# Kernel tuning notes

Hardware: AMD Instinct MI355X
Metric: run time of the kernel (lower is better)

Reference implementation:

```python
import jax, jax.numpy as jnp
import numpy as np

# ---- static config (mirrors ProposalLayerModule param) ----
FEAT_STRIDE = 16
PRE_NMS_TOPN = 6000
POST_NMS_TOPN = 300
NMS_THRESH = 0.7
MIN_SIZE = 16.0
NUM_ANCHORS = 9


def _generate_anchors():
    """Replicates generate_anchors(base_size=16, ratios=[0.5,1,2], scales=[8,16,32])."""
    base = np.array([0.0, 0.0, 15.0, 15.0])
    ratios = np.array([0.5, 1.0, 2.0])
    scales = np.array([8.0, 16.0, 32.0])
    w = base[2] - base[0] + 1.0
    h = base[3] - base[1] + 1.0
    xc = base[0] + 0.5 * (w - 1.0)
    yc = base[1] + 0.5 * (h - 1.0)
    size = w * h
    ws = np.round(np.sqrt(size / ratios))
    hs = np.round(ws * ratios)
    ratio_anchors = np.stack([xc - 0.5 * (ws - 1), yc - 0.5 * (hs - 1),
                              xc + 0.5 * (ws - 1), yc + 0.5 * (hs - 1)], axis=1)
    out = []
    for a in ratio_anchors:
        aw = a[2] - a[0] + 1.0
        ah = a[3] - a[1] + 1.0
        axc = a[0] + 0.5 * (aw - 1.0)
        ayc = a[1] + 0.5 * (ah - 1.0)
        ws2 = aw * scales
        hs2 = ah * scales
        out.append(np.stack([axc - 0.5 * (ws2 - 1), ayc - 0.5 * (hs2 - 1),
                             axc + 0.5 * (ws2 - 1), ayc + 0.5 * (hs2 - 1)], axis=1))
    return np.concatenate(out, axis=0).astype(np.float32)  # (9, 4)

_ANCHORS = _generate_anchors()


def _nms_keep(iou, valid, thresh):
    """Greedy NMS over score-sorted boxes. Returns boolean keep mask."""
    n = iou.shape[0]
    idx = jnp.arange(n)
    def body(i, keep):
        sup = keep[i] & (iou[i] > thresh) & (idx > i)
        return keep & jnp.logical_not(sup)
    return jax.lax.fori_loop(0, n, body, valid)


def setup_inputs() -> dict:
    key = jax.random.key(0)
    k1, k2 = jax.random.split(key)
    H, W = 128, 192
    scores = jax.random.normal(k1, (1, 2 * NUM_ANCHORS, H, W), dtype=jnp.float32)
    # small deltas so exp(dw), exp(dh) stay in a realistic range
    bbox_deltas = jax.random.normal(k2, (1, 4 * NUM_ANCHORS, H, W), dtype=jnp.float32) * 0.1
    im_info = jnp.array([H * FEAT_STRIDE, W * FEAT_STRIDE, 1.0], dtype=jnp.float32)
    return {"scores": scores, "bbox_deltas": bbox_deltas, "im_info": im_info}


def reference(scores, bbox_deltas, im_info):
    A = NUM_ANCHORS
    s = scores[0, A:]                      # (A, H, W) fg scores
    Hf, Wf = s.shape[1], s.shape[2]
    # shifts, matching torch.meshgrid default indexing='ij' (x-major flatten)
    shift_x = jnp.arange(Wf, dtype=jnp.float32) * FEAT_STRIDE
    shift_y = jnp.arange(Hf, dtype=jnp.float32) * FEAT_STRIDE
    sx, sy = jnp.meshgrid(shift_x, shift_y, indexing='ij')   # (W, H)
    shifts = jnp.stack([sx.ravel(), sy.ravel(), sx.ravel(), sy.ravel()], axis=1)  # (K,4)
    anchors = (jnp.asarray(_ANCHORS)[None, :, :] + shifts[:, None, :]).reshape(-1, 4)  # (K*A,4)

    deltas = jnp.transpose(bbox_deltas[0], (1, 2, 0)).reshape(-1, 4)  # (H*W*A,4)
    sc = jnp.transpose(s, (1, 2, 0)).reshape(-1)                      # (H*W*A,)

    # bbox_transform_inv
    widths = anchors[:, 2] - anchors[:, 0] + 1.0
    heights = anchors[:, 3] - anchors[:, 1] + 1.0
    ctr_x = anchors[:, 0] + 0.5 * widths
    ctr_y = anchors[:, 1] + 0.5 * heights
    dx, dy, dw, dh = deltas[:, 0], deltas[:, 1], deltas[:, 2], deltas[:, 3]
    pcx = dx * widths + ctr_x
    pcy = dy * heights + ctr_y
    pw = jnp.exp(dw) * widths
    ph = jnp.exp(dh) * heights
    x1 = pcx - 0.5 * pw
    y1 = pcy - 0.5 * ph
    x2 = pcx + 0.5 * pw
    y2 = pcy + 0.5 * ph

    # clip_boxes
    x1 = jnp.clip(x1, 0.0, im_info[1] - 1.0)
    x2 = jnp.clip(x2, 0.0, im_info[1] - 1.0)
    y1 = jnp.clip(y1, 0.0, im_info[0] - 1.0)
    y2 = jnp.clip(y2, 0.0, im_info[0] - 1.0)
    boxes = jnp.stack([x1, y1, x2, y2], axis=1)

    # _filter_boxes (as a mask, jit-friendly)
    ms = MIN_SIZE * im_info[2]
    valid = ((x2 - x1 + 1.0) >= ms) & ((y2 - y1 + 1.0) >= ms)
    masked_sc = jnp.where(valid, sc, -jnp.inf)

    # sort by score descending + pre_nms_topN
    top_s, top_i = jax.lax.top_k(masked_sc, PRE_NMS_TOPN)
    b = boxes[top_i]                       # (PRE, 4), score-sorted
    vld = jnp.isfinite(top_s)

    # torchvision-style IoU (no +1) + greedy NMS
    area = (b[:, 2] - b[:, 0]) * (b[:, 3] - b[:, 1])
    ix1 = jnp.maximum(b[:, None, 0], b[None, :, 0])
    iy1 = jnp.maximum(b[:, None, 1], b[None, :, 1])
    ix2 = jnp.minimum(b[:, None, 2], b[None, :, 2])
    iy2 = jnp.minimum(b[:, None, 3], b[None, :, 3])
    inter = jnp.clip(ix2 - ix1, 0.0) * jnp.clip(iy2 - iy1, 0.0)
    iou = inter / jnp.maximum(area[:, None] + area[None, :] - inter, 1e-9)
    keep = _nms_keep(iou, vld, NMS_THRESH)

    # first post_nms_topN kept boxes (fixed-size, zero-padded), prepend batch idx 0
    cum = jnp.cumsum(keep.astype(jnp.int32))
    pos = jnp.where(keep & (cum <= POST_NMS_TOPN), cum - 1, POST_NMS_TOPN)
    rows = jnp.concatenate([jnp.zeros((PRE_NMS_TOPN, 1), jnp.float32), b], axis=1)
    out = jnp.zeros((POST_NMS_TOPN + 1, 5), jnp.float32).at[pos].set(rows)[:POST_NMS_TOPN]
    return out
```

## Files before the change

kernel.cpp:

```cpp
#include <hip/hip_runtime.h>

#define NCELL 24576
#define NTOT  221184
#define NBIN13 8192
#define TOPN  6000
#define POSTN 300
#define NPADR 6016
#define NW    94
#define CW    8
#define NCHUNK 12
#define NCB   16
#define SLOT  1024
#define CAP2  (NCB*SLOT)

__global__ void decode_kernel(const float* __restrict__ scores,
                              const float* __restrict__ deltas,
                              const float* __restrict__ iminfo,
                              float4* __restrict__ boxes,
                              unsigned* __restrict__ skeys) {
#pragma clang fp contract(off)
    int c = blockIdx.x * blockDim.x + threadIdx.x;
    if (c >= NCELL) return;
    const float AW[9] = {184.f,368.f,736.f,128.f,256.f,512.f, 88.f,176.f,352.f};
    const float AH[9] = { 96.f,192.f,384.f,128.f,256.f,512.f,176.f,352.f,704.f};
    float sx = (float)((c >> 7) << 4);
    float sy = (float)((c & 127) << 4);
    float imh = iminfo[0], imw = iminfo[1], ims = iminfo[2];
    float xhi = imw - 1.0f, yhi = imh - 1.0f;
    float ms = 16.0f * ims;
    float ctrx = sx + 8.0f, ctry = sy + 8.0f;
    const float* sbase = scores + 9 * NCELL + c;
    const float* dbase = deltas + c;
#pragma unroll
    for (int a = 0; a < 9; ++a) {
        float sc = sbase[a * NCELL];
        float dx = dbase[(4 * a + 0) * NCELL];
        float dy = dbase[(4 * a + 1) * NCELL];
        float dw = dbase[(4 * a + 2) * NCELL];
        float dh = dbase[(4 * a + 3) * NCELL];
        float pcx = dx * AW[a] + ctrx;
        float pcy = dy * AH[a] + ctry;
        float pw = expf(dw) * AW[a];
        float ph = expf(dh) * AH[a];
        float x1 = pcx - 0.5f * pw;
        float y1 = pcy - 0.5f * ph;
        float x2 = pcx + 0.5f * pw;
        float y2 = pcy + 0.5f * ph;
        x1 = fminf(fmaxf(x1, 0.0f), xhi);
        x2 = fminf(fmaxf(x2, 0.0f), xhi);
        y1 = fminf(fmaxf(y1, 0.0f), yhi);
        y2 = fminf(fmaxf(y2, 0.0f), yhi);
        bool valid = ((x2 - x1 + 1.0f) >= ms) && ((y2 - y1 + 1.0f) >= ms);
        unsigned u = __float_as_uint(sc);
        unsigned key = (u & 0x80000000u) ? ~u : (u | 0x80000000u);
        if (!valid) key = 0x007FFFFFu;
        boxes[a * NCELL + c] = make_float4(x1, y1, x2, y2);
        skeys[a * NCELL + c] = key;
    }
}

__global__ __launch_bounds__(1024) void compactT_kernel(const unsigned* __restrict__ skeys,
                                                        unsigned* __restrict__ meta16,
                                                        unsigned long long* __restrict__ cbuf) {
    __shared__ unsigned hist[NBIN13];
    __shared__ unsigned psum[1024];
    __shared__ unsigned csum[256];
    __shared__ unsigned sB, sAbove, sT, sCount;
    int tid = threadIdx.x, bid = blockIdx.x;
    for (int b = tid; b < NBIN13; b += 1024) hist[b] = 0u;
    if (tid == 0) sCount = 0u;
    __syncthreads();
    const uint4* s4 = (const uint4*)skeys;
    for (int q = tid; q < NTOT / 4; q += 1024) {
        uint4 u = s4[q];
        atomicAdd(&hist[u.x >> 19], 1u);
        atomicAdd(&hist[u.y >> 19], 1u);
        atomicAdd(&hist[u.z >> 19], 1u);
        atomicAdd(&hist[u.w >> 19], 1u);
    }
    __syncthreads();
    unsigned s = 0;
#pragma unroll
    for (int q = 0; q < 8; ++q) s += hist[tid * 8 + q];
    psum[tid] = s;
    __syncthreads();
    if (tid < 256)
        csum[tid] = psum[tid * 4] + psum[tid * 4 + 1] + psum[tid * 4 + 2] + psum[tid * 4 + 3];
    __syncthreads();
    if (tid < 64) {
        int lane = tid;
        unsigned c0 = csum[lane * 4 + 0], c1 = csum[lane * 4 + 1];
        unsigned c2 = csum[lane * 4 + 2], c3 = csum[lane * 4 + 3];
        unsigned ls = c0 + c1 + c2 + c3;
        unsigned v = ls;
#pragma unroll
        for (int o = 1; o < 64; o <<= 1) {
            unsigned t = __shfl_down(v, o, 64);
            if (lane + o < 64) v += t;
        }
        unsigned sufExcl = v - ls;
        unsigned a3 = sufExcl;
        unsigned a2 = a3 + c3;
        unsigned a1 = a2 + c2;
        unsigned a0 = a1 + c1;
        if (a0 < TOPN && a0 + c0 >= TOPN) { sB = lane * 4 + 0; sAbove = a0; }
        if (a1 < TOPN && a1 + c1 >= TOPN) { sB = lane * 4 + 1; sAbove = a1; }
        if (a2 < TOPN && a2 + c2 >= TOPN) { sB = lane * 4 + 2; sAbove = a2; }
        if (a3 < TOPN && a3 + c3 >= TOPN) { sB = lane * 4 + 3; sAbove = a3; }
    }
    __syncthreads();
    if (tid < 32) {
        unsigned B = sB, above = sAbove;
        unsigned h = hist[B * 32 + tid];
        unsigned v = h;
#pragma unroll
        for (int o = 1; o < 32; o <<= 1) {
            unsigned t = __shfl_down(v, o, 64);
            if (tid + o < 32) v += t;
        }
        unsigned sufExcl = v - h;
        unsigned ab = above + sufExcl;
        if (ab < TOPN && ab + h >= TOPN) sT = B * 32 + tid;
    }
    __syncthreads();
    unsigned T = sT;
    int base = bid * (NTOT / NCB);
    const uint4* s4b = (const uint4*)(skeys + base);
    for (int q = tid; q < (NTOT / NCB) / 4; q += 1024) {
        uint4 u = s4b[q];
        unsigned k4[4] = {u.x, u.y, u.z, u.w};
#pragma unroll
        for (int k = 0; k < 4; ++k) {
            if ((k4[k] >> 19) >= T) {
                unsigned lp = atomicAdd(&sCount, 1u);
                if (lp < SLOT) {
                    int m = base + 4 * q + k;
                    unsigned n = (unsigned)((m % NCELL) * 9 + (m / NCELL));
                    cbuf[(bid << 10) + lp] =
                        ((unsigned long long)k4[k] << 32) | (unsigned long long)(~n);
                }
            }
        }
    }
    __syncthreads();
    unsigned cnt = sCount; if (cnt > SLOT) cnt = SLOT;
    for (int e = cnt + tid; e < SLOT; e += 1024) cbuf[(bid << 10) + e] = 0ULL;
    if (tid == 0) meta16[bid] = cnt;
}

__global__ __launch_bounds__(256) void rankscatter_kernel(const unsigned long long* __restrict__ cbuf,
                                                          const unsigned* __restrict__ meta16,
                                                          const float4* __restrict__ boxes,
                                                          float4* __restrict__ sortedbox) {
    __shared__ unsigned long long jk[512];
    __shared__ unsigned scnt[NCB];
    int tid = threadIdx.x;
    if (tid < NCB) scnt[tid] = meta16[tid];
    __syncthreads();
    int i = blockIdx.x * 32 + (tid >> 3);
    int slice = tid & 7;
    unsigned long long ki = cbuf[i];
    unsigned cr = 0;
    for (int jt = 0; jt < CAP2 / 512; ++jt) {
        int b = jt >> 1;
        unsigned cb = scnt[b];
        if ((jt & 1) ? (cb <= 512u) : (cb == 0u)) continue;
        __syncthreads();
        for (int q = tid; q < 512; q += 256) jk[q] = cbuf[(jt << 9) + q];
        __syncthreads();
#pragma unroll 8
        for (int j = 0; j < 64; ++j) cr += (jk[slice + (j << 3)] > ki) ? 1u : 0u;
    }
    cr += __shfl_down(cr, 4, 8);
    cr += __shfl_down(cr, 2, 8);
    cr += __shfl_down(cr, 1, 8);
    if (slice == 0 && ki != 0ULL && cr < NPADR) {
        unsigned n = ~(unsigned)ki;
        unsigned m = (n % 9u) * (unsigned)NCELL + (n / 9u);
        sortedbox[cr] = boxes[m];
    }
}

__global__ __launch_bounds__(256) void matrix_kernel(const float4* __restrict__ sortedbox,
                                                     unsigned long long* __restrict__ rowr,
                                                     unsigned long long* __restrict__ diagw,
                                                     unsigned long long* __restrict__ diagT) {
#pragma clang fp contract(off)
    __shared__ float4 jb[256];
    __shared__ float  ja[256];
    int tid = threadIdx.x;
    int lane = tid & 63, wave = tid >> 6;
    int i0 = blockIdx.y << 6;
    int i = i0 + lane;
    int w = (blockIdx.x << 2) + wave;
    int jbase = blockIdx.x << 8;
    unsigned long long word = 0ULL;

    if (jbase + 255 > i0) {
        int jg = jbase + tid;
        float4 v = (jg < NPADR) ? sortedbox[jg] : make_float4(0.f, 0.f, 0.f, 0.f);
        jb[tid] = v;
        ja[tid] = (v.z - v.x) * (v.w - v.y);
        __syncthreads();
        if (w < NW && ((w << 6) + 63) > i) {
            float4 bi = sortedbox[i];
            float ai = (bi.z - bi.x) * (bi.w - bi.y);
            int jl0 = wave << 6;
            int jg0 = (w << 6);
#pragma unroll 8
            for (int j = 0; j < 64; ++j) {
                float4 bj = jb[jl0 + j];
                float aj = ja[jl0 + j];
                float iw = fminf(bi.z, bj.z) - fmaxf(bi.x, bj.x);
                float ih = fminf(bi.w, bj.w) - fmaxf(bi.y, bj.y);
                iw = fmaxf(iw, 0.0f);
                ih = fmaxf(ih, 0.0f);
                float inter = iw * ih;
                float denom = fmaxf(ai + aj - inter, 1e-9f);
                bool sup = (jg0 + j > i) && (inter / denom > 0.7f);
                word |= (unsigned long long)sup << j;
            }
        }
    }
    if (w < NW) {
        rowr[(size_t)i * NW + w] = word;
        if ((i >> 9) == (w >> 3))
            diagw[((size_t)w << 9) + (i & 511)] = word;
        if (w == (i >> 6)) {
            unsigned long long col = 0ULL;
#pragma unroll
            for (int jbit = 0; jbit < 64; ++jbit) {
                unsigned long long m = __ballot((word >> jbit) & 1ULL);
                if (lane == jbit) col = m;
            }
            diagT[((size_t)w << 6) + lane] = col;
        }
    }
}

__global__ __launch_bounds__(256) void scan_kernel(const unsigned long long* __restrict__ rowr,
                                                   const unsigned long long* __restrict__ diagw,
                                                   const unsigned long long* __restrict__ diagT,
                                                   const float4* __restrict__ sortedbox,
                                                   float* __restrict__ out) {
    __shared__ __align__(16) unsigned long long cblk[2][CW * 512];
    __shared__ unsigned long long ldsT[2][CW * 64];
    __shared__ unsigned long long gm[128];
    __shared__ int keptArr[POSTN];
    __shared__ int s_kept, s_done;
    int tid = threadIdx.x;
    int lane = tid & 63, wave = tid >> 6;

    if (tid < 128) gm[tid] = (tid == 93) ? ~((1ULL << 48) - 1) : 0ULL;
    if (tid == 0) { s_kept = 0; s_done = 0; }
    for (int e = tid; e < CW * 512; e += 256) cblk[0][e] = diagw[e];
    for (int e = tid; e < CW * 64; e += 256) ldsT[0][e] = diagT[e];
    __syncthreads();

    int keptPrev = 0;
    for (int c = 0; c < NCHUNK; ++c) {
        int buf = c & 1, nbuf = buf ^ 1;
        int wbase = c * CW;
        if (wave == 0) {
            unsigned long long dgT[CW];
#pragma unroll
            for (int q = 0; q < CW; ++q) dgT[q] = ldsT[buf][(q << 6) + lane];
            unsigned long long lowmask = (1ULL << lane) - 1ULL;
            int kept = s_kept;
            int done = 0;
            for (int q = 0; q < CW && wbase + q < NW; ++q) {
                int w = wbase + q;
                unsigned long long live = ~gm[w];
                if (w == NW - 1) live &= (1ULL << 48) - 1;
                if (!live) continue;
                bool alive = (live >> lane) & 1ULL;
                unsigned long long x = live;
                for (;;) {
                    bool sup = (dgT[q] & x & lowmask) != 0ULL;
                    unsigned long long xn = __ballot(alive && !sup);
                    if (xn == x) break;
                    x = xn;
                }
                unsigned long long kb = x;
                if (kb) {
                    int nk = __popcll(kb);
                    int myr = __popcll(kb & lowmask);
                    if (((kb >> lane) & 1ULL) && (kept + myr < POSTN))
                        keptArr[kept + myr] = (w << 6) + lane;
                    kept += nk;
                    if (kept >= POSTN) { kept = POSTN; done = 1; }
                }
                if (kb && !done && q < CW - 1) {
                    bool act = (lane > q) && (lane < CW);
                    int base = (lane << 9) + (q << 6);
                    unsigned long long acc = 0ULL;
                    unsigned long long t = kb;
                    while (t) {
                        int b0 = __ffsll((unsigned long long)t) - 1; t &= t - 1;
                        int b1 = 0, b2 = 0, b3 = 0, nb = 1;
                        if (t) { b1 = __ffsll((unsigned long long)t) - 1; t &= t - 1; nb = 2; }
                        if (t) { b2 = __ffsll((unsigned long long)t) - 1; t &= t - 1; nb = 3; }
                        if (t) { b3 = __ffsll((unsigned long long)t) - 1; t &= t - 1; nb = 4; }
                        unsigned long long r0 = act ? cblk[buf][base + b0] : 0ULL;
                        unsigned long long r1 = (act && nb > 1) ? cblk[buf][base + b1] : 0ULL;
                        unsigned long long r2 = (act && nb > 2) ? cblk[buf][base + b2] : 0ULL;
                        unsigned long long r3 = (act && nb > 3) ? cblk[buf][base + b3] : 0ULL;
                        acc |= (r0 | r1) | (r2 | r3);
                    }
                    if (act && acc) atomicOr(&gm[wbase + lane], acc);
                }
                if (done) break;
            }
            if (lane == 0) { s_kept = kept; s_done = done; }
        } else if (c + 1 < NCHUNK) {
            int t = tid - 64;
            int wb2 = wbase + CW;
            int rb2 = wb2 << 6;
            for (int e = t; e < CW * 512; e += 192) {
                int q = e >> 9, r = e & 511;
                cblk[nbuf][e] = (wb2 + q < NW && rb2 + r < NPADR)
                    ? diagw[((size_t)(wb2 + q) << 9) + r] : 0ULL;
            }
            for (int e = t; e < CW * 64; e += 192) {
                int q = e >> 6;
                ldsT[nbuf][e] = (wb2 + q < NW) ? diagT[((size_t)wb2 << 6) + e] : 0ULL;
            }
        }
        __syncthreads();
        int keptNow = s_kept;
        bool fin = (s_done != 0) || (c == NCHUNK - 1);
        if (fin) break;
        {
            int w = tid & 127, g = tid >> 7;
            if (w < NW && w >= wbase) {
                unsigned long long a = 0ULL;
                int s = keptPrev + g;
                for (; s + 14 < keptNow; s += 16) {
                    size_t r0 = (size_t)keptArr[s]      * NW;
                    size_t r1 = (size_t)keptArr[s + 2]  * NW;
                    size_t r2 = (size_t)keptArr[s + 4]  * NW;
                    size_t r3 = (size_t)keptArr[s + 6]  * NW;
                    size_t r4 = (size_t)keptArr[s + 8]  * NW;
                    size_t r5 = (size_t)keptArr[s + 10] * NW;
                    size_t r6 = (size_t)keptArr[s + 12] * NW;
                    size_t r7 = (size_t)keptArr[s + 14] * NW;
                    unsigned long long x0 = rowr[r0 + w];
                    unsigned long long x1 = rowr[r1 + w];
                    unsigned long long x2 = rowr[r2 + w];
                    unsigned long long x3 = rowr[r3 + w];
                    unsigned long long x4 = rowr[r4 + w];
                    unsigned long long x5 = rowr[r5 + w];
                    unsigned long long x6 = rowr[r6 + w];
                    unsigned long long x7 = rowr[r7 + w];
                    a |= (x0 | x1) | (x2 | x3) | (x4 | x5) | (x6 | x7);
                }
                for (; s < keptNow; s += 2)
                    a |= rowr[(size_t)keptArr[s] * NW + w];
                if (a) atomicOr(&gm[w], a);
            }
        }
        keptPrev = keptNow;
        __syncthreads();
    }
    __syncthreads();

    int kept = s_kept;
    for (int k = tid; k < POSTN; k += 256) {
        float4 bb = make_float4(0.f, 0.f, 0.f, 0.f);
        if (k < kept) bb = sortedbox[keptArr[k]];
        out[k * 5 + 0] = 0.0f;
        out[k * 5 + 1] = bb.x;
        out[k * 5 + 2] = bb.y;
        out[k * 5 + 3] = bb.z;
        out[k * 5 + 4] = bb.w;
    }
}

extern "C" void kernel_launch(void* const* d_in, const int* in_sizes, int n_in,
                              void* d_out, int out_size, void* d_ws, size_t ws_size,
                              hipStream_t stream) {
    const float* scores = (const float*)d_in[0];
    const float* deltas = (const float*)d_in[1];
    const float* iminfo = (const float*)d_in[2];
    char* w = (char*)d_ws;
    float4*   boxes = (float4*)w;
    unsigned* skeys = (unsigned*)(w + 3538944);
    unsigned long long* rowr = (unsigned long long*)w;
    unsigned* meta16 = (unsigned*)(w + 4786176);
    unsigned long long* cbuf = (unsigned long long*)(w + 4786240);
    float4* sortedbox = (float4*)(w + 4917312);
    unsigned long long* diagw = (unsigned long long*)(w + 5013568);
    unsigned long long* diagT = (unsigned long long*)(w + 5398592);
    float* out = (float*)d_out;

    decode_kernel<<<NCELL / 256, 256, 0, stream>>>(scores, deltas, iminfo, boxes, skeys);
    compactT_kernel<<<NCB, 1024, 0, stream>>>(skeys, meta16, cbuf);
    rankscatter_kernel<<<CAP2 / 32, 256, 0, stream>>>(cbuf, meta16, boxes, sortedbox);
    matrix_kernel<<<dim3(24, 94), 256, 0, stream>>>(sortedbox, rowr, diagw, diagT);
    scan_kernel<<<1, 256, 0, stream>>>(rowr, diagw, diagT, sortedbox, out);
}
```

Measured before the change: 161.0 us.

## Overlap NMS mask OR-reduction with chunk scan and halve histogram key reads

The scan kernel grows to 512 threads. Four extra waves OR the previous chunk's kept rows into the far columns of the global suppression mask while wave 0 scans the current chunk. After the barrier, only the next chunk's columns are updated synchronously, so less of the serial mask update sits on the critical path. Decode also writes a 16-bit copy of the sort keys, which the histogram pass reads to halve its traffic. The matrix kernel skips storing row words below the diagonal. The added atomics and the extra key write may cost more than they save.

```diff
diff --git a/kernel.cpp b/kernel.cpp
--- a/kernel.cpp
+++ b/kernel.cpp
@@ -17,7 +17,8 @@
                               const float* __restrict__ deltas,
                               const float* __restrict__ iminfo,
                               float4* __restrict__ boxes,
-                              unsigned* __restrict__ skeys) {
+                              unsigned* __restrict__ skeys,
+                              unsigned short* __restrict__ skeys16) {
 #pragma clang fp contract(off)
     int c = blockIdx.x * blockDim.x + threadIdx.x;
     if (c >= NCELL) return;
@@ -56,10 +57,12 @@
         if (!valid) key = 0x007FFFFFu;
         boxes[a * NCELL + c] = make_float4(x1, y1, x2, y2);
         skeys[a * NCELL + c] = key;
+        skeys16[a * NCELL + c] = (unsigned short)(key >> 16);
     }
 }
 
 __global__ __launch_bounds__(1024) void compactT_kernel(const unsigned* __restrict__ skeys,
+                                                        const unsigned short* __restrict__ skeys16,
                                                         unsigned* __restrict__ meta16,
                                                         unsigned long long* __restrict__ cbuf) {
     __shared__ unsigned hist[NBIN13];
@@ -70,12 +73,16 @@
     for (int b = tid; b < NBIN13; b += 1024) hist[b] = 0u;
     if (tid == 0) sCount = 0u;
     __syncthreads();
-    const uint4* s4 = (const uint4*)skeys;
-    for (int q = tid; q < NTOT / 4; q += 1024) {
-        uint4 u = s4[q];
+    const uint4* s16 = (const uint4*)skeys16;
+    for (int q = tid; q < NTOT / 8; q += 1024) {
+        uint4 u = s16[q];
+        atomicAdd(&hist[(u.x & 0xFFFFu) >> 3], 1u);
         atomicAdd(&hist[u.x >> 19], 1u);
+        atomicAdd(&hist[(u.y & 0xFFFFu) >> 3], 1u);
         atomicAdd(&hist[u.y >> 19], 1u);
+        atomicAdd(&hist[(u.z & 0xFFFFu) >> 3], 1u);
         atomicAdd(&hist[u.z >> 19], 1u);
+        atomicAdd(&hist[(u.w & 0xFFFFu) >> 3], 1u);
         atomicAdd(&hist[u.w >> 19], 1u);
     }
     __syncthreads();
@@ -223,7 +230,8 @@
         }
     }
     if (w < NW) {
-        rowr[(size_t)i * NW + w] = word;
+        if (w >= (i >> 6))
+            rowr[(size_t)i * NW + w] = word;
         if ((i >> 9) == (w >> 3))
             diagw[((size_t)w << 9) + (i & 511)] = word;
         if (w == (i >> 6)) {
@@ -238,7 +246,7 @@
     }
 }
 
-__global__ __launch_bounds__(256) void scan_kernel(const unsigned long long* __restrict__ rowr,
+__global__ __launch_bounds__(512) void scan_kernel(const unsigned long long* __restrict__ rowr,
                                                    const unsigned long long* __restrict__ diagw,
                                                    const unsigned long long* __restrict__ diagT,
                                                    const float4* __restrict__ sortedbox,
@@ -253,11 +261,12 @@
 
     if (tid < 128) gm[tid] = (tid == 93) ? ~((1ULL << 48) - 1) : 0ULL;
     if (tid == 0) { s_kept = 0; s_done = 0; }
-    for (int e = tid; e < CW * 512; e += 256) cblk[0][e] = diagw[e];
-    for (int e = tid; e < CW * 64; e += 256) ldsT[0][e] = diagT[e];
+    for (int e = tid; e < CW * 512; e += 512) cblk[0][e] = diagw[e];
+    for (int e = tid; e < CW * 64; e += 512) ldsT[0][e] = diagT[e];
     __syncthreads();
 
     int keptPrev = 0;
+    int keptPrev2 = 0;
     for (int c = 0; c < NCHUNK; ++c) {
         int buf = c & 1, nbuf = buf ^ 1;
         int wbase = c * CW;
@@ -312,60 +321,59 @@
                 if (done) break;
             }
             if (lane == 0) { s_kept = kept; s_done = done; }
-        } else if (c + 1 < NCHUNK) {
-            int t = tid - 64;
-            int wb2 = wbase + CW;
-            int rb2 = wb2 << 6;
-            for (int e = t; e < CW * 512; e += 192) {
-                int q = e >> 9, r = e & 511;
-                cblk[nbuf][e] = (wb2 + q < NW && rb2 + r < NPADR)
-                    ? diagw[((size_t)(wb2 + q) << 9) + r] : 0ULL;
-            }
-            for (int e = t; e < CW * 64; e += 192) {
-                int q = e >> 6;
-                ldsT[nbuf][e] = (wb2 + q < NW) ? diagT[((size_t)wb2 << 6) + e] : 0ULL;
+        } else if (wave < 4) {
+            if (c + 1 < NCHUNK) {
+                int t = tid - 64;
+                int wb2 = wbase + CW;
+                int rb2 = wb2 << 6;
+                for (int e = t; e < CW * 512; e += 192) {
+                    int q = e >> 9, r = e & 511;
+                    cblk[nbuf][e] = (wb2 + q < NW && rb2 + r < NPADR)
+                        ? diagw[((size_t)(wb2 + q) << 9) + r] : 0ULL;
+                }
+                for (int e = t; e < CW * 64; e += 192) {
+                    int q = e >> 6;
+                    ldsT[nbuf][e] = (wb2 + q < NW) ? diagT[((size_t)wb2 << 6) + e] : 0ULL;
+                }
+            }
+        } else {
+            int nw2 = NW - (wbase + CW);
+            int nr2 = keptPrev - keptPrev2;
+            if (c > 0 && nr2 > 0 && nw2 > 0) {
+                int t = tid - 256;
+                int tot = nr2 * nw2;
+                for (int idx = t; idx < tot; idx += 256) {
+                    int s = idx / nw2, wo = idx - s * nw2;
+                    int row = keptArr[keptPrev2 + s];
+                    unsigned long long v = rowr[(size_t)row * NW + (wbase + CW) + wo];
+                    if (v) atomicOr(&gm[wbase + CW + wo], v);
+                }
             }
         }
         __syncthreads();
         int keptNow = s_kept;
         bool fin = (s_done != 0) || (c == NCHUNK - 1);
+        if (!fin && keptNow > keptPrev) {
+            int w1 = wbase + CW;
+            int nw1 = NW - w1; if (nw1 > CW) nw1 = CW;
+            int wo = tid & 7;
+            for (int s = keptPrev + (tid >> 3); s < keptNow; s += 64) {
+                if (wo < nw1) {
+                    int row = keptArr[s];
+                    unsigned long long v = rowr[(size_t)row * NW + w1 + wo];
+                    if (v) atomicOr(&gm[w1 + wo], v);
+                }
+            }
+        }
+        keptPrev2 = keptPrev;
+        keptPrev = keptNow;
         if (fin) break;
-        {
-            int w = tid & 127, g = tid >> 7;
-            if (w < NW && w >= wbase) {
-                unsigned long long a = 0ULL;
-                int s = keptPrev + g;
-                for (; s + 14 < keptNow; s += 16) {
-                    size_t r0 = (size_t)keptArr[s]      * NW;
-                    size_t r1 = (size_t)keptArr[s + 2]  * NW;
-                    size_t r2 = (size_t)keptArr[s + 4]  * NW;
-                    size_t r3 = (size_t)keptArr[s + 6]  * NW;
-                    size_t r4 = (size_t)keptArr[s + 8]  * NW;
-                    size_t r5 = (size_t)keptArr[s + 10] * NW;
-                    size_t r6 = (size_t)keptArr[s + 12] * NW;
-                    size_t r7 = (size_t)keptArr[s + 14] * NW;
-                    unsigned long long x0 = rowr[r0 + w];
-                    unsigned long long x1 = rowr[r1 + w];
-                    unsigned long long x2 = rowr[r2 + w];
-                    unsigned long long x3 = rowr[r3 + w];
-                    unsigned long long x4 = rowr[r4 + w];
-                    unsigned long long x5 = rowr[r5 + w];
-                    unsigned long long x6 = rowr[r6 + w];
-                    unsigned long long x7 = rowr[r7 + w];
-                    a |= (x0 | x1) | (x2 | x3) | (x4 | x5) | (x6 | x7);
-                }
-                for (; s < keptNow; s += 2)
-                    a |= rowr[(size_t)keptArr[s] * NW + w];
-                if (a) atomicOr(&gm[w], a);
-            }
-        }
-        keptPrev = keptNow;
         __syncthreads();
     }
     __syncthreads();
 
     int kept = s_kept;
-    for (int k = tid; k < POSTN; k += 256) {
+    for (int k = tid; k < POSTN; k += 512) {
         float4 bb = make_float4(0.f, 0.f, 0.f, 0.f);
         if (k < kept) bb = sortedbox[keptArr[k]];
         out[k * 5 + 0] = 0.0f;
@@ -391,11 +399,12 @@
     float4* sortedbox = (float4*)(w + 4917312);
     unsigned long long* diagw = (unsigned long long*)(w + 5013568);
     unsigned long long* diagT = (unsigned long long*)(w + 5398592);
+    unsigned short* skeys16 = (unsigned short*)(w + 5446720);
     float* out = (float*)d_out;
 
-    decode_kernel<<<NCELL / 256, 256, 0, stream>>>(scores, deltas, iminfo, boxes, skeys);
-    compactT_kernel<<<NCB, 1024, 0, stream>>>(skeys, meta16, cbuf);
+    decode_kernel<<<NCELL / 256, 256, 0, stream>>>(scores, deltas, iminfo, boxes, skeys, skeys16);
+    compactT_kernel<<<NCB, 1024, 0, stream>>>(skeys, skeys16, meta16, cbuf);
     rankscatter_kernel<<<CAP2 / 32, 256, 0, stream>>>(cbuf, meta16, boxes, sortedbox);
     matrix_kernel<<<dim3(24, 94), 256, 0, stream>>>(sortedbox, rowr, diagw, diagT);
-    scan_kernel<<<1, 256, 0, stream>>>(rowr, diagw, diagT, sortedbox, out);
-}
+    scan_kernel<<<1, 512, 0, stream>>>(rowr, diagw, diagT, sortedbox, out);
+}
```

Measured after the change: 156.9 us. -2.5%, faster.
